# Kernel optimization log

Hardware: AMD Instinct MI355X
Metric: run time of the kernel (lower is better)

Reference implementation:

```python
import jax, jax.numpy as jnp
import numpy as np

B, S, D, E, K = 2, 4096, 1024, 8, 2

def setup_inputs() -> dict:
    key = jax.random.key(0)
    k1, k2, k3, k4, k5 = jax.random.split(key, 5)
    x = jax.random.normal(k1, (B, S, D), dtype=jnp.float32)
    expert_weights = jax.random.uniform(k2, (B, S, K), dtype=jnp.float32)
    top_k_indices = jax.random.randint(k3, (B, S, K), 0, E, dtype=jnp.int32)
    W = jax.random.normal(k4, (E, D, D), dtype=jnp.float32) * (1.0 / np.sqrt(D))
    b = jax.random.normal(k5, (E, D), dtype=jnp.float32) * 0.01
    return {"x": x, "expert_weights": expert_weights,
            "top_k_indices": top_k_indices, "W": W, "b": b}

def reference(x, expert_weights, top_k_indices, W, b):
    # Dense all-expert linear: [B,S,E,Dout]
    expert_outputs = jnp.einsum('bsd,edf->bsef', x, W) + b  # bias broadcasts over b,s
    # Gather the top-k expert outputs per token: [B,S,K,Dout]
    gathered = jnp.take_along_axis(expert_outputs, top_k_indices[:, :, :, None], axis=2)
    # Weighted combine over k
    output = jnp.sum(expert_weights[:, :, :, None] * gathered, axis=2)
    return output
```

## Files before the change

### kernel.cpp

```cpp
#include <hip/hip_runtime.h>
#include <hip/hip_bf16.h>
#include <cstdio>
#include <cstdint>

static constexpr int TOK = 8192;
static constexpr int DIM = 1024;
static constexpr int NEXP = 8;
static constexpr int NGRP = 16;

typedef unsigned short u16;
typedef unsigned int u32;

using floatx4 = __attribute__((ext_vector_type(4))) float;
using bf16x8  = __attribute__((ext_vector_type(8))) __bf16;


__device__ __forceinline__ u16 f2bf(float f) {
  union { float f; u32 u; } v; v.f = f;
  u32 r = v.u + 0x7fffu + ((v.u >> 16) & 1u);
  return (u16)(r >> 16);
}

__device__ __forceinline__ float bf2f(u16 b) {
  union { u32 u; float f; } v; v.u = (u32)b << 16;
  return v.f;
}

__device__ __forceinline__ void gload_lds16(const void* g, void* l) {
  __builtin_amdgcn_global_load_lds(
      (const __attribute__((address_space(1))) void*)g,
      (__attribute__((address_space(3))) void*)l,
      16, 0, 0);
}

__global__ __launch_bounds__(1024)
void trans_prep_kernel(const float* __restrict__ W, u16* __restrict__ wt,
                       const int* __restrict__ idx, const float* __restrict__ ew,
                       int* __restrict__ meta, int* __restrict__ tileMap,
                       int* __restrict__ tokList, float* __restrict__ wList,
                       int* __restrict__ posOf) {
  const int bid = blockIdx.x;
  const int tid = threadIdx.x;
  if (bid < 2048) {
    __shared__ u16 tile4[4][32][33];
    const int sub = tid >> 8;
    const int t4 = bid * 4 + sub;
    const int e = t4 >> 10;
    const int f0 = ((t4 >> 5) & 31) * 32, d0 = (t4 & 31) * 32;
    const float* src = W + ((size_t)e << 20);
    u16* dst = wt + ((size_t)e << 20);
    const int tl = tid & 255;
    const int tx = tl & 31, ty = tl >> 5;
#pragma unroll
    for (int j = 0; j < 4; ++j) {
      int d = d0 + ty + 8 * j;
      tile4[sub][ty + 8 * j][tx] = f2bf(src[(size_t)d * DIM + f0 + tx]);
    }
    __syncthreads();
#pragma unroll
    for (int j = 0; j < 4; ++j) {
      int f = f0 + ty + 8 * j;
      dst[(size_t)f * DIM + d0 + tx] = tile4[sub][tx][ty + 8 * j];
    }
  } else {
    __shared__ int cnt2[16][NGRP];
    __shared__ int cur2[16][NGRP];
    __shared__ int tot[NGRP], offS[NGRP], tbase[NGRP];
    const int wid = tid >> 6;
    if (tid < 16 * NGRP) ((int*)cnt2)[tid] = 0;
    __syncthreads();
    int gl[16];
#pragma unroll
    for (int j = 0; j < 16; ++j) {
      int i = tid + 1024 * j;
      int g = ((i & 1) << 3) | idx[i];
      gl[j] = g;
      atomicAdd(&cnt2[wid][g], 1);
    }
    __syncthreads();
    if (tid < NGRP) {
      int s = 0;
      for (int w = 0; w < 16; ++w) { cur2[w][tid] = s; s += cnt2[w][tid]; }
      tot[tid] = s;
    }
    __syncthreads();
    if (tid == 0) {
      int run = 0, t = 0, tk0 = 0;
      for (int g = 0; g < NGRP; ++g) {
        offS[g] = run; tbase[g] = t;
        t += (tot[g] + 127) >> 7;
        if (g == NEXP - 1) tk0 = t;
        run += tot[g];
      }
      meta[48] = t;
      meta[49] = tk0;
    }
    __syncthreads();
    if (tid < NGRP) {
      meta[tid] = tot[tid];
      meta[16 + tid] = offS[tid];
      int b = tbase[tid], n = (tot[tid] + 127) >> 7;
      for (int m0 = 0; m0 < n; ++m0) tileMap[b + m0] = (tid << 12) | m0;
    }
    if (tid < 16 * NGRP) {
      int w = tid >> 4, g = tid & 15;
      cur2[w][g] += offS[g];
    }
    __syncthreads();
#pragma unroll
    for (int j = 0; j < 16; ++j) {
      int i = tid + 1024 * j;
      int pos = atomicAdd(&cur2[wid][gl[j]], 1);
      tokList[pos] = i >> 1;
      wList[pos] = ew[i];
      posOf[i] = pos;
    }
  }
}

__global__ __launch_bounds__(256)
void gather_x_kernel(const float* __restrict__ x, const int* __restrict__ posOf,
                     u16* __restrict__ Abuf) {
  const int t = blockIdx.x, tid = threadIdx.x;
  float4 v = reinterpret_cast<const float4*>(x + ((size_t)t << 10))[tid];
  ushort4 o;
  o.x = f2bf(v.x); o.y = f2bf(v.y); o.z = f2bf(v.z); o.w = f2bf(v.w);
  const int p0 = posOf[2 * t], p1 = posOf[2 * t + 1];
  reinterpret_cast<ushort4*>(Abuf + ((size_t)p0 << 10))[tid] = o;
  reinterpret_cast<ushort4*>(Abuf + ((size_t)p1 << 10))[tid] = o;
}

__global__ __launch_bounds__(256, 4)
void moe_gemm_kernel(const u16* __restrict__ Abuf, const u16* __restrict__ wt,
                     const float* __restrict__ bias, const int* __restrict__ tokList,
                     const float* __restrict__ wList, const int* __restrict__ meta,
                     const int* __restrict__ tileMap, float* __restrict__ out,
                     u16* __restrict__ cbufA, u16* __restrict__ cbufB, int mode,
                     int pass) {
  constexpr int BM = 128, BN = 128, BK = 64;
  const int chunk = gridDim.y;
  int lin = blockIdx.y * 8 + blockIdx.x;
  int swz = (lin & 7) * chunk + (lin >> 3);
  int tileIdx = swz >> 3, nt = swz & 7;

  int tBase = 0, tEnd = meta[48];
  const int tilesK0 = meta[49];
  if (mode == 0) { if (pass == 0) tEnd = tilesK0; else tBase = tilesK0; }
  tileIdx += tBase;
  if (tileIdx >= tEnd) return;

  const int tm = tileMap[tileIdx];
  const int g = tm >> 12, m0 = tm & 0xfff;
  const int e = g & (NEXP - 1);
  const int nrem = meta[g] - m0 * BM;
  const int listBase = meta[16 + g] + m0 * BM;

  __shared__ __align__(16) u16 As[BM * BK];
  __shared__ __align__(16) u16 Bs[BN * BK];

  const int tid = threadIdx.x;
  const int rowA = tid >> 3;
  const int chnk = tid & 7;
  const int csw  = chnk ^ (rowA & 7);
  const u16* wb = wt + ((size_t)e << 20);
  const u16* ab = Abuf + ((size_t)listBase << 10);

  const int wid = tid >> 6, lane = tid & 63;
  const int wm = (wid >> 1) * 64, wn = (wid & 1) * 64;
  const int lr = lane & 15, lg = lane >> 4;
  const int rx = lr & 7;

  floatx4 acc[4][4];
#pragma unroll
  for (int i = 0; i < 4; ++i)
#pragma unroll
    for (int j = 0; j < 4; ++j) acc[i][j] = (floatx4){0.f, 0.f, 0.f, 0.f};

  for (int kt = 0; kt < DIM / BK; ++kt) {
    __syncthreads();
#pragma unroll
    for (int r = 0; r < 4; ++r) {
      const int row = rowA + 32 * r;
      gload_lds16(ab + ((size_t)row << 10) + kt * BK + csw * 8,
                  &As[row * BK + chnk * 8]);
    }
#pragma unroll
    for (int r = 0; r < 4; ++r) {
      const int row = rowA + 32 * r;
      gload_lds16(wb + ((size_t)(nt * BN + row) << 10) + kt * BK + csw * 8,
                  &Bs[row * BK + chnk * 8]);
    }
    asm volatile("s_waitcnt vmcnt(0)" ::: "memory");
    __syncthreads();

#pragma unroll
    for (int ks = 0; ks < 2; ++ks) {
      bf16x8 av[4], bv[4];
#pragma unroll
      for (int mi = 0; mi < 4; ++mi)
        av[mi] = *reinterpret_cast<const bf16x8*>(
            &As[(wm + mi * 16 + lr) * BK + (((ks * 4 + lg) ^ rx)) * 8]);
#pragma unroll
      for (int ni = 0; ni < 4; ++ni)
        bv[ni] = *reinterpret_cast<const bf16x8*>(
            &Bs[(wn + ni * 16 + lr) * BK + (((ks * 4 + lg) ^ rx)) * 8]);
#pragma unroll
      for (int mi = 0; mi < 4; ++mi)
#pragma unroll
        for (int ni = 0; ni < 4; ++ni)
          acc[mi][ni] = __builtin_amdgcn_mfma_f32_16x16x32_bf16(av[mi], bv[ni], acc[mi][ni], 0, 0, 0);
    }
  }

  u16* cb = nullptr;
  bool rmw = false, f32out = false;
  if (mode == 2)      cb = (g < NEXP) ? cbufA : cbufB;
  else if (mode == 1) { if (g < NEXP) f32out = true; else cb = cbufA; }
  else                { f32out = true; rmw = (pass == 1); }
  const float* bp = bias + e * DIM;
#pragma unroll
  for (int mi = 0; mi < 4; ++mi) {
#pragma unroll
    for (int r = 0; r < 4; ++r) {
      const int rl = wm + mi * 16 + lg * 4 + r;
      if (rl < nrem) {
        const int   tok = tokList[listBase + rl];
        const float w   = wList[listBase + rl];
        const size_t rowOff = (size_t)tok << 10;
#pragma unroll
        for (int ni = 0; ni < 4; ++ni) {
          const int col = nt * BN + wn + ni * 16 + lr;
          const float v = w * (acc[mi][ni][r] + bp[col]);
          if (f32out) { if (rmw) out[rowOff + col] += v; else out[rowOff + col] = v; }
          else        cb[rowOff + col] = f2bf(v);
        }
      }
    }
  }
}

__global__ __launch_bounds__(256)
void combine2_kernel(float* __restrict__ out, const u16* __restrict__ cbufA,
                     const u16* __restrict__ cbufB) {
  const int p = blockIdx.x * 256 + threadIdx.x;
  uint4 ca = reinterpret_cast<const uint4*>(cbufA)[p];
  uint4 cb = reinterpret_cast<const uint4*>(cbufB)[p];
  float4 r0, r1;
  r0.x = bf2f((u16)(ca.x & 0xffff)) + bf2f((u16)(cb.x & 0xffff));
  r0.y = bf2f((u16)(ca.x >> 16))    + bf2f((u16)(cb.x >> 16));
  r0.z = bf2f((u16)(ca.y & 0xffff)) + bf2f((u16)(cb.y & 0xffff));
  r0.w = bf2f((u16)(ca.y >> 16))    + bf2f((u16)(cb.y >> 16));
  r1.x = bf2f((u16)(ca.z & 0xffff)) + bf2f((u16)(cb.z & 0xffff));
  r1.y = bf2f((u16)(ca.z >> 16))    + bf2f((u16)(cb.z >> 16));
  r1.z = bf2f((u16)(ca.w & 0xffff)) + bf2f((u16)(cb.w & 0xffff));
  r1.w = bf2f((u16)(ca.w >> 16))    + bf2f((u16)(cb.w >> 16));
  float4* o4 = reinterpret_cast<float4*>(out) + 2 * (size_t)p;
  o4[0] = r0; o4[1] = r1;
}

__global__ __launch_bounds__(256)
void combine_kernel(float* __restrict__ out, const u16* __restrict__ cbuf) {
  const int p = blockIdx.x * 256 + threadIdx.x;
  uint4 c = reinterpret_cast<const uint4*>(cbuf)[p];
  float4* o4 = reinterpret_cast<float4*>(out) + 2 * (size_t)p;
  float4 a = o4[0], b = o4[1];
  a.x += bf2f((u16)(c.x & 0xffff)); a.y += bf2f((u16)(c.x >> 16));
  a.z += bf2f((u16)(c.y & 0xffff)); a.w += bf2f((u16)(c.y >> 16));
  b.x += bf2f((u16)(c.z & 0xffff)); b.y += bf2f((u16)(c.z >> 16));
  b.z += bf2f((u16)(c.w & 0xffff)); b.w += bf2f((u16)(c.w >> 16));
  o4[0] = a; o4[1] = b;
}

extern "C" void kernel_launch(void* const* d_in, const int* in_sizes, int n_in,
                              void* d_out, int out_size, void* d_ws, size_t ws_size,
                              hipStream_t stream) {
  const float* x    = (const float*)d_in[0];
  const float* ew   = (const float*)d_in[1];
  const int*   idx  = (const int*)d_in[2];
  const float* W    = (const float*)d_in[3];
  const float* bias = (const float*)d_in[4];
  float* out = (float*)d_out;

  char* ws = (char*)d_ws;
  u16*   Abuf  = (u16*)ws;
  u16*   wtp   = (u16*)(ws + ((size_t)32 << 20));
  u16*   cbufA = (u16*)(ws + ((size_t)48 << 20));
  u16*   cbufB = (u16*)(ws + ((size_t)64 << 20));

  const size_t tailSz = (size_t)(194 << 10);
  const size_t need0 = ((size_t)48 << 20) + tailSz;
  const size_t need1 = ((size_t)64 << 20) + tailSz;
  const size_t need2 = ((size_t)80 << 20) + tailSz;
  if (ws_size < need0) {
    fprintf(stderr, "kernel_launch: ws_size %zu < needed %zu\n", ws_size, need0);
    return;
  }
  const int mode = (ws_size >= need2) ? 2 : (ws_size >= need1) ? 1 : 0;
  char* tail = ws + ((mode == 2) ? ((size_t)80 << 20)
                                 : (mode == 1) ? ((size_t)64 << 20)
                                               : ((size_t)48 << 20));
  int*   tokList = (int*)tail;
  float* wList   = (float*)(tail + (64 << 10));
  int*   posOf   = (int*)(tail + (128 << 10));
  int*   meta    = (int*)(tail + (192 << 10));
  int*   tileMap = (int*)(tail + (193 << 10));

  trans_prep_kernel<<<2049, 1024, 0, stream>>>(W, wtp, idx, ew, meta, tileMap,
                                               tokList, wList, posOf);
  gather_x_kernel<<<TOK, 256, 0, stream>>>(x, posOf, Abuf);

  if (mode == 2) {
    moe_gemm_kernel<<<dim3(8, 144), 256, 0, stream>>>(
        Abuf, wtp, bias, tokList, wList, meta, tileMap, out, cbufA, cbufB, 2, 0);
    combine2_kernel<<<TOK * DIM / 8 / 256, 256, 0, stream>>>(out, cbufA, cbufB);
  } else if (mode == 1) {
    moe_gemm_kernel<<<dim3(8, 144), 256, 0, stream>>>(
        Abuf, wtp, bias, tokList, wList, meta, tileMap, out, cbufA, nullptr, 1, 0);
    combine_kernel<<<TOK * DIM / 8 / 256, 256, 0, stream>>>(out, cbufA);
  } else {
    moe_gemm_kernel<<<dim3(8, 72), 256, 0, stream>>>(
        Abuf, wtp, bias, tokList, wList, meta, tileMap, out, nullptr, nullptr, 0, 0);
    moe_gemm_kernel<<<dim3(8, 72), 256, 0, stream>>>(
        Abuf, wtp, bias, tokList, wList, meta, tileMap, out, nullptr, nullptr, 0, 1);
  }
}
```

Baseline: 116.8 us.

## Double-buffer LDS tiles with BK=32 to overlap global loads and MFMA

The main GEMM loop now uses two LDS buffers with a K-tile of 32 and issues the next tile's global-to-LDS loads before computing on the current tile. This is meant to hide global load latency behind MFMA work instead of waiting on every tile before computing. LDS footprint stays the same, but there are twice as many K iterations, each with a full vmcnt wait and barrier, and a narrower 4-chunk XOR swizzle that may raise LDS bank conflicts.

```diff
diff --git a/kernel.cpp b/kernel.cpp
--- a/kernel.cpp
+++ b/kernel.cpp
@@ -137,7 +137,8 @@
                      const int* __restrict__ tileMap, float* __restrict__ out,
                      u16* __restrict__ cbufA, u16* __restrict__ cbufB, int mode,
                      int pass) {
-  constexpr int BM = 128, BN = 128, BK = 64;
+  constexpr int BM = 128, BN = 128, BK = 32;
+  constexpr int NKT = DIM / BK;
   const int chunk = gridDim.y;
   int lin = blockIdx.y * 8 + blockIdx.x;
   int swz = (lin & 7) * chunk + (lin >> 3);
@@ -155,20 +156,20 @@
   const int nrem = meta[g] - m0 * BM;
   const int listBase = meta[16 + g] + m0 * BM;
 
-  __shared__ __align__(16) u16 As[BM * BK];
-  __shared__ __align__(16) u16 Bs[BN * BK];
+  __shared__ __align__(16) u16 As[2][BM * BK];
+  __shared__ __align__(16) u16 Bs[2][BN * BK];
 
   const int tid = threadIdx.x;
-  const int rowA = tid >> 3;
-  const int chnk = tid & 7;
-  const int csw  = chnk ^ (rowA & 7);
+  const int rowA = tid >> 2;
+  const int chnk = tid & 3;
+  const int csw  = chnk ^ (rowA & 3);
   const u16* wb = wt + ((size_t)e << 20);
   const u16* ab = Abuf + ((size_t)listBase << 10);
 
   const int wid = tid >> 6, lane = tid & 63;
   const int wm = (wid >> 1) * 64, wn = (wid & 1) * 64;
   const int lr = lane & 15, lg = lane >> 4;
-  const int rx = lr & 7;
+  const int rx = lr & 3;
 
   floatx4 acc[4][4];
 #pragma unroll
@@ -176,46 +177,51 @@
 #pragma unroll
     for (int j = 0; j < 4; ++j) acc[i][j] = (floatx4){0.f, 0.f, 0.f, 0.f};
 
-  for (int kt = 0; kt < DIM / BK; ++kt) {
-    __syncthreads();
-#pragma unroll
-    for (int r = 0; r < 4; ++r) {
-      const int row = rowA + 32 * r;
-      gload_lds16(ab + ((size_t)row << 10) + kt * BK + csw * 8,
-                  &As[row * BK + chnk * 8]);
-    }
-#pragma unroll
-    for (int r = 0; r < 4; ++r) {
-      const int row = rowA + 32 * r;
-      gload_lds16(wb + ((size_t)(nt * BN + row) << 10) + kt * BK + csw * 8,
-                  &Bs[row * BK + chnk * 8]);
-    }
+#pragma unroll
+  for (int r = 0; r < 2; ++r) {
+    const int row = rowA + 64 * r;
+    gload_lds16(ab + ((size_t)row << 10) + csw * 8, &As[0][row * BK + chnk * 8]);
+    gload_lds16(wb + ((size_t)(nt * BN + row) << 10) + csw * 8,
+                &Bs[0][row * BK + chnk * 8]);
+  }
+  asm volatile("s_waitcnt vmcnt(0)" ::: "memory");
+  __syncthreads();
+
+  for (int kt = 0; kt < NKT; ++kt) {
+    const int cb = kt & 1;
+    if (kt < NKT - 1) {
+      const int koff = (kt + 1) * BK;
+#pragma unroll
+      for (int r = 0; r < 2; ++r) {
+        const int row = rowA + 64 * r;
+        gload_lds16(ab + ((size_t)row << 10) + koff + csw * 8,
+                    &As[cb ^ 1][row * BK + chnk * 8]);
+        gload_lds16(wb + ((size_t)(nt * BN + row) << 10) + koff + csw * 8,
+                    &Bs[cb ^ 1][row * BK + chnk * 8]);
+      }
+    }
+    bf16x8 av[4], bv[4];
+#pragma unroll
+    for (int mi = 0; mi < 4; ++mi)
+      av[mi] = *reinterpret_cast<const bf16x8*>(
+          &As[cb][(wm + mi * 16 + lr) * BK + ((lg ^ rx)) * 8]);
+#pragma unroll
+    for (int ni = 0; ni < 4; ++ni)
+      bv[ni] = *reinterpret_cast<const bf16x8*>(
+          &Bs[cb][(wn + ni * 16 + lr) * BK + ((lg ^ rx)) * 8]);
+#pragma unroll
+    for (int mi = 0; mi < 4; ++mi)
+#pragma unroll
+      for (int ni = 0; ni < 4; ++ni)
+        acc[mi][ni] = __builtin_amdgcn_mfma_f32_16x16x32_bf16(av[mi], bv[ni], acc[mi][ni], 0, 0, 0);
     asm volatile("s_waitcnt vmcnt(0)" ::: "memory");
     __syncthreads();
-
-#pragma unroll
-    for (int ks = 0; ks < 2; ++ks) {
-      bf16x8 av[4], bv[4];
-#pragma unroll
-      for (int mi = 0; mi < 4; ++mi)
-        av[mi] = *reinterpret_cast<const bf16x8*>(
-            &As[(wm + mi * 16 + lr) * BK + (((ks * 4 + lg) ^ rx)) * 8]);
-#pragma unroll
-      for (int ni = 0; ni < 4; ++ni)
-        bv[ni] = *reinterpret_cast<const bf16x8*>(
-            &Bs[(wn + ni * 16 + lr) * BK + (((ks * 4 + lg) ^ rx)) * 8]);
-#pragma unroll
-      for (int mi = 0; mi < 4; ++mi)
-#pragma unroll
-        for (int ni = 0; ni < 4; ++ni)
-          acc[mi][ni] = __builtin_amdgcn_mfma_f32_16x16x32_bf16(av[mi], bv[ni], acc[mi][ni], 0, 0, 0);
-    }
-  }
-
-  u16* cb = nullptr;
+  }
+
+  u16* cbp = nullptr;
   bool rmw = false, f32out = false;
-  if (mode == 2)      cb = (g < NEXP) ? cbufA : cbufB;
-  else if (mode == 1) { if (g < NEXP) f32out = true; else cb = cbufA; }
+  if (mode == 2)      cbp = (g < NEXP) ? cbufA : cbufB;
+  else if (mode == 1) { if (g < NEXP) f32out = true; else cbp = cbufA; }
   else                { f32out = true; rmw = (pass == 1); }
   const float* bp = bias + e * DIM;
 #pragma unroll
@@ -232,7 +238,7 @@
           const int col = nt * BN + wn + ni * 16 + lr;
           const float v = w * (acc[mi][ni][r] + bp[col]);
           if (f32out) { if (rmw) out[rowOff + col] += v; else out[rowOff + col] = v; }
-          else        cb[rowOff + col] = f2bf(v);
+          else        cbp[rowOff + col] = f2bf(v);
         }
       }
     }
```

After: 128.8 us. 10.3% more time.
